# Kernel optimization log

Measured on AMD Instinct MI355X. Metric: run time of the kernel, lower is better.

## Reference

```python
import jax, jax.numpy as jnp
import numpy as np

B, S, D_MODEL, D_QK, D_VO = 4, 2048, 1024, 128, 128
NEG = -1.0e9


def setup_inputs() -> dict:
    key = jax.random.key(0)
    k1, k2, k3, k4, k5 = jax.random.split(key, 5)
    enc = jax.random.normal(k1, (B, S, D_MODEL), dtype=jnp.float32)
    # causal mask: True means masked (masked_fill), broadcast over batch
    causal = jnp.triu(jnp.ones((S, S), dtype=bool), k=1)
    mask = jnp.broadcast_to(causal, (B, S, S))
    scale = 0.02
    W_q = jax.random.normal(k2, (D_MODEL, D_QK), dtype=jnp.float32) * scale
    W_k = jax.random.normal(k3, (D_MODEL, D_QK), dtype=jnp.float32) * scale
    W_v = jax.random.normal(k4, (D_MODEL, D_VO), dtype=jnp.float32) * scale
    W_o = jax.random.normal(k5, (D_VO, D_MODEL), dtype=jnp.float32) * scale
    return {"encodings": enc, "mask": mask, "W_q": W_q, "W_k": W_k, "W_v": W_v, "W_o": W_o}


def reference(encodings, mask, W_q, W_k, W_v, W_o):
    # q,k: [B,S,d_qk]; v: [B,S,d_vo]
    q = jnp.einsum('bsd,de->bse', encodings, W_q)
    k = jnp.einsum('bsd,de->bse', encodings, W_k)
    v = jnp.einsum('bsd,de->bse', encodings, W_v)
    sims = jnp.einsum('bqe,bke->bqk', q, k) / jnp.asarray(D_QK ** 0.5, q.dtype)
    sims = jnp.where(mask, jnp.asarray(NEG, sims.dtype), sims)
    attn = jax.nn.softmax(sims, axis=-1)  # [B,S,S]
    scores = jnp.einsum('bqk,bke->bqe', attn, v)  # [B,S,d_vo]
    return jnp.einsum('bse,ed->bsd', scores, W_o)  # [B,S,d_model]
```

## Files before the change

### kernel.cpp

```cpp
#include <hip/hip_runtime.h>
#include <hip/hip_bf16.h>
#include <stdint.h>

typedef __attribute__((ext_vector_type(8))) short short8;
typedef __attribute__((ext_vector_type(4))) float floatx4;

using bf16 = __hip_bfloat16;

#define SCALE_L2 0.12751793359133147f

__device__ inline unsigned short f2b(float f) {
    bf16 h = __float2bfloat16(f);
    return *(unsigned short*)&h;
}

__global__ __launch_bounds__(256) void prep_all(const float4* __restrict__ enc4,
                                                ushort4* __restrict__ encb4,
                                                const float* __restrict__ Wq,
                                                const float* __restrict__ Wk,
                                                const float* __restrict__ Wv,
                                                const float* __restrict__ Wo,
                                                bf16* __restrict__ Wqkvt,
                                                bf16* __restrict__ Wot) {
    int bx = blockIdx.x;
    if (bx < 8192) {
        int i = bx * 256 + threadIdx.x;
        float4 v = enc4[i];
        ushort4 o;
        o.x = f2b(v.x); o.y = f2b(v.y); o.z = f2b(v.z); o.w = f2b(v.w);
        encb4[i] = o;
    } else {
        int idx = (bx - 8192) * 256 + threadIdx.x;
        int sel = idx >> 17;
        int i = idx & 131071;
        if (sel < 3) {
            const float* W = (sel == 0) ? Wq : (sel == 1) ? Wk : Wv;
            int r = i >> 7, c = i & 127;
            Wqkvt[(size_t)(sel * 128 + c) * 1024 + r] = __float2bfloat16(W[i]);
        } else {
            int r = i >> 10, c = i & 1023;
            Wot[(size_t)c * 128 + r] = __float2bfloat16(Wo[i]);
        }
    }
}

__global__ __launch_bounds__(256) void gemm_qkv64(const bf16* __restrict__ A,
                                                  const bf16* __restrict__ Bt,
                                                  bf16* __restrict__ Qb,
                                                  bf16* __restrict__ Kb,
                                                  bf16* __restrict__ Vtb) {
    __shared__ bf16 As[64 * 40];
    __shared__ bf16 Bs[64 * 40];

    const int tid = threadIdx.x;
    const int m0 = blockIdx.x * 64;
    const int brow0 = blockIdx.y * 64;
    const int proj = brow0 >> 7;
    const int colb = brow0 & 127;
    const int w = tid >> 6, lane = tid & 63;
    const int wm = (w >> 1) * 32, wn = (w & 1) * 32;
    const int quad = lane >> 4, l16 = lane & 15;

    const int ra = tid >> 2, ca = (tid & 3) * 8;

    floatx4 acc[2][2];
#pragma unroll
    for (int i = 0; i < 2; i++)
#pragma unroll
        for (int j = 0; j < 2; j++) acc[i][j] = (floatx4){0.f, 0.f, 0.f, 0.f};

    int4 pa = *(const int4*)&A[(size_t)(m0 + ra) * 1024 + ca];
    int4 pb = *(const int4*)&Bt[(size_t)(brow0 + ra) * 1024 + ca];

    for (int k0 = 0; k0 < 1024; k0 += 32) {
        __syncthreads();
        *(int4*)&As[ra * 40 + ca] = pa;
        *(int4*)&Bs[ra * 40 + ca] = pb;
        __syncthreads();

        if (k0 + 32 < 1024) {
            pa = *(const int4*)&A[(size_t)(m0 + ra) * 1024 + k0 + 32 + ca];
            pb = *(const int4*)&Bt[(size_t)(brow0 + ra) * 1024 + k0 + 32 + ca];
        }

        short8 a[2], b[2];
#pragma unroll
        for (int mt = 0; mt < 2; mt++)
            a[mt] = *(const short8*)&As[(wm + mt * 16 + l16) * 40 + quad * 8];
#pragma unroll
        for (int nt = 0; nt < 2; nt++)
            b[nt] = *(const short8*)&Bs[(wn + nt * 16 + l16) * 40 + quad * 8];
#pragma unroll
        for (int mt = 0; mt < 2; mt++)
#pragma unroll
            for (int nt = 0; nt < 2; nt++)
                acc[mt][nt] = __builtin_amdgcn_mfma_f32_16x16x32_bf16(a[mt], b[nt], acc[mt][nt], 0, 0, 0);
    }

#pragma unroll
    for (int mt = 0; mt < 2; mt++)
#pragma unroll
        for (int nt = 0; nt < 2; nt++)
#pragma unroll
            for (int r = 0; r < 4; r++) {
                int row = m0 + wm + mt * 16 + quad * 4 + r;
                int col = colb + wn + nt * 16 + l16;
                bf16 h = __float2bfloat16(acc[mt][nt][r]);
                if (proj == 0) {
                    Qb[(size_t)row * 128 + col] = h;
                } else if (proj == 1) {
                    Kb[(size_t)row * 128 + col] = h;
                } else {
                    int bb = row >> 11, ss = row & 2047;
                    Vtb[(size_t)bb * 262144 + (size_t)col * 2048 + ss] = h;
                }
            }
}

__global__ __launch_bounds__(256) void gemm_out(const bf16* __restrict__ A,
                                                const bf16* __restrict__ Bt,
                                                float* __restrict__ C) {
    __shared__ bf16 As[64 * 40];
    __shared__ bf16 Bs[128 * 40];

    const int tid = threadIdx.x;
    const int m0 = blockIdx.x * 64;
    const int n0 = blockIdx.y * 128;
    const int w = tid >> 6, lane = tid & 63;
    const int wm = (w >> 1) * 32, wn = (w & 1) * 64;
    const int quad = lane >> 4, l16 = lane & 15;

    const int ra = tid >> 2, ca = (tid & 3) * 8;
    const int rb0 = tid >> 2, rb1 = (tid + 256) >> 2;

    floatx4 acc[2][4];
#pragma unroll
    for (int i = 0; i < 2; i++)
#pragma unroll
        for (int j = 0; j < 4; j++) acc[i][j] = (floatx4){0.f, 0.f, 0.f, 0.f};

    int4 pa  = *(const int4*)&A[(size_t)(m0 + ra) * 128 + ca];
    int4 pb0 = *(const int4*)&Bt[(size_t)(n0 + rb0) * 128 + ca];
    int4 pb1 = *(const int4*)&Bt[(size_t)(n0 + rb1) * 128 + ca];

    for (int k0 = 0; k0 < 128; k0 += 32) {
        __syncthreads();
        *(int4*)&As[ra * 40 + ca] = pa;
        *(int4*)&Bs[rb0 * 40 + ca] = pb0;
        *(int4*)&Bs[rb1 * 40 + ca] = pb1;
        __syncthreads();

        if (k0 + 32 < 128) {
            pa  = *(const int4*)&A[(size_t)(m0 + ra) * 128 + k0 + 32 + ca];
            pb0 = *(const int4*)&Bt[(size_t)(n0 + rb0) * 128 + k0 + 32 + ca];
            pb1 = *(const int4*)&Bt[(size_t)(n0 + rb1) * 128 + k0 + 32 + ca];
        }

        short8 a[2], b[4];
#pragma unroll
        for (int mt = 0; mt < 2; mt++)
            a[mt] = *(const short8*)&As[(wm + mt * 16 + l16) * 40 + quad * 8];
#pragma unroll
        for (int nt = 0; nt < 4; nt++)
            b[nt] = *(const short8*)&Bs[(wn + nt * 16 + l16) * 40 + quad * 8];
#pragma unroll
        for (int mt = 0; mt < 2; mt++)
#pragma unroll
            for (int nt = 0; nt < 4; nt++)
                acc[mt][nt] = __builtin_amdgcn_mfma_f32_16x16x32_bf16(a[mt], b[nt], acc[mt][nt], 0, 0, 0);
    }

#pragma unroll
    for (int mt = 0; mt < 2; mt++)
#pragma unroll
        for (int nt = 0; nt < 4; nt++)
#pragma unroll
            for (int r = 0; r < 4; r++) {
                int row = m0 + wm + mt * 16 + quad * 4 + r;
                int col = n0 + wn + nt * 16 + l16;
                C[(size_t)row * 1024 + col] = acc[mt][nt][r];
            }
}

__global__ __launch_bounds__(256) void flash_split(const bf16* __restrict__ Q,
                                                   const bf16* __restrict__ K,
                                                   const bf16* __restrict__ Vt,
                                                   float* __restrict__ Op,
                                                   float2* __restrict__ Ml) {
    __shared__ bf16 Ps[4 * 16 * 72];

    const int tid = threadIdx.x;
    const int b = blockIdx.x >> 5;
    const int qt = blockIdx.x & 31;
    const int ks = blockIdx.y;
    const int q0 = qt * 64;
    const int w = tid >> 6, lane = tid & 63;
    const int quad = lane >> 4, l16 = lane & 15;

    const int ntiles = qt + 1;
    const int per = (ntiles + 3) >> 2;
    const int start = ks * per;
    const int end = min(start + per, ntiles);

    const int qrow = q0 + w * 16 + l16;
    const bf16* Qrow = &Q[((size_t)b * 2048 + qrow) * 128];
    short8 qf[4];
#pragma unroll
    for (int k4 = 0; k4 < 4; k4++)
        qf[k4] = *(const short8*)&Qrow[k4 * 32 + quad * 8];

    const bf16* Kb = &K[(size_t)b * 2048 * 128];
    const bf16* Vb = &Vt[(size_t)b * 262144];

    float m_run = -1.0e30f, l_run = 0.f;
    floatx4 o[8];
#pragma unroll
    for (int d = 0; d < 8; d++) o[d] = (floatx4){0.f, 0.f, 0.f, 0.f};

    for (int kt = start; kt < end; kt++) {
        const bf16* Kt = Kb + (size_t)(kt * 64) * 128;
        const bf16* Vtt = Vb + kt * 64;

        floatx4 s_acc[4];
#pragma unroll
        for (int nt = 0; nt < 4; nt++) {
            s_acc[nt] = (floatx4){0.f, 0.f, 0.f, 0.f};
#pragma unroll
            for (int k4 = 0; k4 < 4; k4++) {
                short8 kf = *(const short8*)&Kt[(size_t)(nt * 16 + l16) * 128 + k4 * 32 + quad * 8];
                s_acc[nt] = __builtin_amdgcn_mfma_f32_16x16x32_bf16(kf, qf[k4], s_acc[nt], 0, 0, 0);
            }
        }

        float sv[4][4];
#pragma unroll
        for (int nt = 0; nt < 4; nt++)
#pragma unroll
            for (int r = 0; r < 4; r++) {
                float s = s_acc[nt][r] * SCALE_L2;
                if (kt == qt) {
                    int kcol = kt * 64 + nt * 16 + quad * 4 + r;
                    if (kcol > qrow) s = -1.0e9f;
                }
                sv[nt][r] = s;
            }

        float t0 = fmaxf(fmaxf(sv[0][0], sv[0][1]), fmaxf(sv[0][2], sv[0][3]));
        float t1 = fmaxf(fmaxf(sv[1][0], sv[1][1]), fmaxf(sv[1][2], sv[1][3]));
        float t2 = fmaxf(fmaxf(sv[2][0], sv[2][1]), fmaxf(sv[2][2], sv[2][3]));
        float t3 = fmaxf(fmaxf(sv[3][0], sv[3][1]), fmaxf(sv[3][2], sv[3][3]));
        float tmax = fmaxf(fmaxf(t0, t1), fmaxf(t2, t3));
        tmax = fmaxf(tmax, __shfl_xor(tmax, 16));
        tmax = fmaxf(tmax, __shfl_xor(tmax, 32));

        float mnew = fmaxf(m_run, tmax);
        float alpha = exp2f(m_run - mnew);
        m_run = mnew;

        float rsum = 0.f;
#pragma unroll
        for (int nt = 0; nt < 4; nt++)
#pragma unroll
            for (int r = 0; r < 4; r++) {
                float p = exp2f(sv[nt][r] - mnew);
                sv[nt][r] = p;
                rsum += p;
            }
        rsum += __shfl_xor(rsum, 16);
        rsum += __shfl_xor(rsum, 32);
        l_run = l_run * alpha + rsum;

#pragma unroll
        for (int nt = 0; nt < 4; nt++) {
            ushort4 pk;
            pk.x = f2b(sv[nt][0]); pk.y = f2b(sv[nt][1]);
            pk.z = f2b(sv[nt][2]); pk.w = f2b(sv[nt][3]);
            *(ushort4*)&Ps[w * 1152 + l16 * 72 + nt * 16 + quad * 4] = pk;
        }

#pragma unroll
        for (int d = 0; d < 8; d++) {
            o[d][0] *= alpha; o[d][1] *= alpha; o[d][2] *= alpha; o[d][3] *= alpha;
        }

        short8 pf[2];
#pragma unroll
        for (int k2 = 0; k2 < 2; k2++)
            pf[k2] = *(const short8*)&Ps[w * 1152 + l16 * 72 + k2 * 32 + quad * 8];
#pragma unroll
        for (int d = 0; d < 8; d++)
#pragma unroll
            for (int k2 = 0; k2 < 2; k2++) {
                short8 vf = *(const short8*)&Vtt[(size_t)(d * 16 + l16) * 2048 + k2 * 32 + quad * 8];
                o[d] = __builtin_amdgcn_mfma_f32_16x16x32_bf16(vf, pf[k2], o[d], 0, 0, 0);
            }
    }

    const size_t orow = (size_t)ks * 8192 + b * 2048 + qrow;
#pragma unroll
    for (int d = 0; d < 8; d++) {
        float4 v = {o[d][0], o[d][1], o[d][2], o[d][3]};
        *(float4*)&Op[orow * 128 + d * 16 + quad * 4] = v;
    }
    if (lane < 16) Ml[orow] = make_float2(m_run, l_run);
}

__global__ __launch_bounds__(256) void flash_merge(const float* __restrict__ Op,
                                                   const float2* __restrict__ Ml,
                                                   bf16* __restrict__ Sc) {
    int idx = blockIdx.x * 256 + threadIdx.x;
    int row = idx >> 5, dg = (idx & 31) * 4;

    float2 ml[4];
#pragma unroll
    for (int s = 0; s < 4; s++) ml[s] = Ml[(size_t)s * 8192 + row];
    float M = fmaxf(fmaxf(ml[0].x, ml[1].x), fmaxf(ml[2].x, ml[3].x));
    float L = 0.f, wgt[4];
#pragma unroll
    for (int s = 0; s < 4; s++) {
        wgt[s] = exp2f(ml[s].x - M);
        L += ml[s].y * wgt[s];
    }
    float4 acc = {0.f, 0.f, 0.f, 0.f};
#pragma unroll
    for (int s = 0; s < 4; s++) {
        float4 v = *(const float4*)&Op[((size_t)s * 8192 + row) * 128 + dg];
        acc.x += v.x * wgt[s]; acc.y += v.y * wgt[s];
        acc.z += v.z * wgt[s]; acc.w += v.w * wgt[s];
    }
    float inv = 1.0f / L;
    ushort4 o;
    o.x = f2b(acc.x * inv); o.y = f2b(acc.y * inv);
    o.z = f2b(acc.z * inv); o.w = f2b(acc.w * inv);
    *(ushort4*)&Sc[(size_t)row * 128 + dg] = o;
}

extern "C" void kernel_launch(void* const* d_in, const int* in_sizes, int n_in,
                              void* d_out, int out_size, void* d_ws, size_t ws_size,
                              hipStream_t stream) {
    const float* enc = (const float*)d_in[0];
    const float* Wq = (const float*)d_in[2];
    const float* Wk = (const float*)d_in[3];
    const float* Wv = (const float*)d_in[4];
    const float* Wo = (const float*)d_in[5];
    float* out = (float*)d_out;

    const size_t MB = 1024 * 1024;
    char* ws = (char*)d_ws;
    bf16*   encb  = (bf16*)(ws);
    float*  Op    = (float*)(ws);
    bf16*   Qb    = (bf16*)(ws + 16 * MB);
    bf16*   Kb    = (bf16*)(ws + 18 * MB);
    bf16*   Vtb   = (bf16*)(ws + 20 * MB);
    bf16*   Scb   = (bf16*)(ws + 22 * MB);
    bf16*   Wqkvt = (bf16*)(ws + 24 * MB);
    bf16*   Wot   = (bf16*)(ws + 24 * MB + 768 * 1024);
    float2* Ml    = (float2*)(ws + 25 * MB);

    prep_all<<<10240, 256, 0, stream>>>((const float4*)enc, (ushort4*)encb,
                                        Wq, Wk, Wv, Wo, Wqkvt, Wot);

    dim3 blk(256);
    gemm_qkv64<<<dim3(128, 6), blk, 0, stream>>>(encb, Wqkvt, Qb, Kb, Vtb);

    flash_split<<<dim3(128, 4), blk, 0, stream>>>(Qb, Kb, Vtb, Op, Ml);
    flash_merge<<<1024, blk, 0, stream>>>(Op, Ml, Scb);

    gemm_out<<<dim3(128, 8), blk, 0, stream>>>(Scb, Wot, out);
}
```

Baseline: 222.0 us.

## Rebalance flash split-K work, stage K/V in LDS, widen QKV GEMM tiles

The flash kernel now splits the causal work into fixed 4-tile chunks per query tile, giving 576 balanced blocks instead of a 128x4 grid with uneven per-split counts. K and V tiles are staged through shared memory with register prefetch instead of being read directly from global memory. Partial outputs are stored in bf16 to halve merge traffic, and the merge loops over a variable number of chunks. The QKV GEMM uses 64x128 tiles with direct global-to-LDS loads, which drops the register double buffering and LDS padding and may add bank conflicts and precision loss in the partial sums.

Result: faster. 210.9 us (-5.0%).

```diff
diff --git a/kernel.cpp b/kernel.cpp
--- a/kernel.cpp
+++ b/kernel.cpp
@@ -12,6 +12,17 @@
 __device__ inline unsigned short f2b(float f) {
     bf16 h = __float2bfloat16(f);
     return *(unsigned short*)&h;
+}
+__device__ inline float b2f(unsigned short u) {
+    union { unsigned int i; float f; } v;
+    v.i = ((unsigned int)u) << 16;
+    return v.f;
+}
+
+__device__ __forceinline__ void gll16(const bf16* g, bf16* l) {
+    __builtin_amdgcn_global_load_lds((__attribute__((address_space(1))) void*)g,
+                                     (__attribute__((address_space(3))) void*)l,
+                                     16, 0, 0);
 }
 
 __global__ __launch_bounds__(256) void prep_all(const float4* __restrict__ enc4,
@@ -44,71 +55,67 @@
     }
 }
 
-__global__ __launch_bounds__(256) void gemm_qkv64(const bf16* __restrict__ A,
-                                                  const bf16* __restrict__ Bt,
-                                                  bf16* __restrict__ Qb,
-                                                  bf16* __restrict__ Kb,
-                                                  bf16* __restrict__ Vtb) {
-    __shared__ bf16 As[64 * 40];
-    __shared__ bf16 Bs[64 * 40];
+__global__ __launch_bounds__(256) void gemm_qkv(const bf16* __restrict__ A,
+                                                const bf16* __restrict__ Bt,
+                                                bf16* __restrict__ Qb,
+                                                bf16* __restrict__ Kb,
+                                                bf16* __restrict__ Vtb) {
+    __shared__ bf16 As[64 * 32];
+    __shared__ bf16 Bs[128 * 32];
 
     const int tid = threadIdx.x;
     const int m0 = blockIdx.x * 64;
-    const int brow0 = blockIdx.y * 64;
-    const int proj = brow0 >> 7;
-    const int colb = brow0 & 127;
+    const int nsel = blockIdx.y;
+    const int brow0 = nsel * 128;
     const int w = tid >> 6, lane = tid & 63;
-    const int wm = (w >> 1) * 32, wn = (w & 1) * 32;
+    const int wm = (w >> 1) * 32, wn = (w & 1) * 64;
     const int quad = lane >> 4, l16 = lane & 15;
 
-    const int ra = tid >> 2, ca = (tid & 3) * 8;
-
-    floatx4 acc[2][2];
+    const int ar = tid >> 2, akq = (tid & 3) * 8;
+    const int br1 = (tid + 256) >> 2;
+    bf16* As_w  = &As[w * 512];
+    bf16* Bs_w0 = &Bs[w * 512];
+    bf16* Bs_w1 = &Bs[2048 + w * 512];
+
+    floatx4 acc[2][4];
 #pragma unroll
     for (int i = 0; i < 2; i++)
 #pragma unroll
-        for (int j = 0; j < 2; j++) acc[i][j] = (floatx4){0.f, 0.f, 0.f, 0.f};
-
-    int4 pa = *(const int4*)&A[(size_t)(m0 + ra) * 1024 + ca];
-    int4 pb = *(const int4*)&Bt[(size_t)(brow0 + ra) * 1024 + ca];
+        for (int j = 0; j < 4; j++) acc[i][j] = (floatx4){0.f, 0.f, 0.f, 0.f};
 
     for (int k0 = 0; k0 < 1024; k0 += 32) {
         __syncthreads();
-        *(int4*)&As[ra * 40 + ca] = pa;
-        *(int4*)&Bs[ra * 40 + ca] = pb;
-        __syncthreads();
-
-        if (k0 + 32 < 1024) {
-            pa = *(const int4*)&A[(size_t)(m0 + ra) * 1024 + k0 + 32 + ca];
-            pb = *(const int4*)&Bt[(size_t)(brow0 + ra) * 1024 + k0 + 32 + ca];
-        }
-
-        short8 a[2], b[2];
+        gll16(&A[(size_t)(m0 + ar) * 1024 + k0 + akq], As_w);
+        gll16(&Bt[(size_t)(brow0 + ar) * 1024 + k0 + akq], Bs_w0);
+        gll16(&Bt[(size_t)(brow0 + br1) * 1024 + k0 + akq], Bs_w1);
+        __syncthreads();
+
+        short8 a[2], b[4];
 #pragma unroll
         for (int mt = 0; mt < 2; mt++)
-            a[mt] = *(const short8*)&As[(wm + mt * 16 + l16) * 40 + quad * 8];
-#pragma unroll
-        for (int nt = 0; nt < 2; nt++)
-            b[nt] = *(const short8*)&Bs[(wn + nt * 16 + l16) * 40 + quad * 8];
+            a[mt] = *(const short8*)&As[(wm + mt * 16 + l16) * 32 + quad * 8];
+#pragma unroll
+        for (int nt = 0; nt < 4; nt++)
+            b[nt] = *(const short8*)&Bs[(wn + nt * 16 + l16) * 32 + quad * 8];
 #pragma unroll
         for (int mt = 0; mt < 2; mt++)
 #pragma unroll
-            for (int nt = 0; nt < 2; nt++)
+            for (int nt = 0; nt < 4; nt++)
                 acc[mt][nt] = __builtin_amdgcn_mfma_f32_16x16x32_bf16(a[mt], b[nt], acc[mt][nt], 0, 0, 0);
     }
 
 #pragma unroll
     for (int mt = 0; mt < 2; mt++)
 #pragma unroll
-        for (int nt = 0; nt < 2; nt++)
+        for (int nt = 0; nt < 4; nt++)
 #pragma unroll
             for (int r = 0; r < 4; r++) {
                 int row = m0 + wm + mt * 16 + quad * 4 + r;
-                int col = colb + wn + nt * 16 + l16;
+                int col = wn + nt * 16 + l16;
                 bf16 h = __float2bfloat16(acc[mt][nt][r]);
-                if (proj == 0) {
+                if (nsel == 0) {
                     Qb[(size_t)row * 128 + col] = h;
-                } else if (proj == 1) {
+                } else if (nsel == 1) {
                     Kb[(size_t)row * 128 + col] = h;
                 } else {
                     int bb = row >> 11, ss = row & 2047;
@@ -185,22 +192,29 @@
 __global__ __launch_bounds__(256) void flash_split(const bf16* __restrict__ Q,
                                                    const bf16* __restrict__ K,
                                                    const bf16* __restrict__ Vt,
-                                                   float* __restrict__ Op,
+                                                   bf16* __restrict__ Opb,
                                                    float2* __restrict__ Ml) {
+    __shared__ bf16 Ks[64 * 136];
+    __shared__ bf16 Vs[128 * 72];
     __shared__ bf16 Ps[4 * 16 * 72];
 
     const int tid = threadIdx.x;
-    const int b = blockIdx.x >> 5;
-    const int qt = blockIdx.x & 31;
-    const int ks = blockIdx.y;
+    const int x = blockIdx.x;
+    const int b = x / 144;
+    const int id = x - b * 144;
+    const int g = (id >= 112) ? 7 : (id >= 84) ? 6 : (id >= 60) ? 5 : (id >= 40) ? 4
+                : (id >= 24) ? 3 : (id >= 12) ? 2 : (id >= 4) ? 1 : 0;
+    const int nc = g + 1;
+    const int local = id - 2 * g * nc;
+    const int qi = local / nc;
+    const int c = local - qi * nc;
+    const int qt = 4 * g + qi;
     const int q0 = qt * 64;
+    const int start = 4 * c;
+    const int end = min(start + 4, qt + 1);
+
     const int w = tid >> 6, lane = tid & 63;
     const int quad = lane >> 4, l16 = lane & 15;
-
-    const int ntiles = qt + 1;
-    const int per = (ntiles + 3) >> 2;
-    const int start = ks * per;
-    const int end = min(start + per, ntiles);
 
     const int qrow = q0 + w * 16 + l16;
     const bf16* Qrow = &Q[((size_t)b * 2048 + qrow) * 128];
@@ -209,17 +223,39 @@
     for (int k4 = 0; k4 < 4; k4++)
         qf[k4] = *(const short8*)&Qrow[k4 * 32 + quad * 8];
 
-    const bf16* Kb = &K[(size_t)b * 2048 * 128];
-    const bf16* Vb = &Vt[(size_t)b * 262144];
-
     float m_run = -1.0e30f, l_run = 0.f;
     floatx4 o[8];
 #pragma unroll
     for (int d = 0; d < 8; d++) o[d] = (floatx4){0.f, 0.f, 0.f, 0.f};
 
+    int4 kreg[4], vreg[4];
+    const int sr[4]  = {(tid + 0) >> 4, (tid + 256) >> 4, (tid + 512) >> 4, (tid + 768) >> 4};
+    const int scg    = (tid & 15) * 8;
+    const int sr2[4] = {(tid + 0) >> 3, (tid + 256) >> 3, (tid + 512) >> 3, (tid + 768) >> 3};
+    const int scg2   = (tid & 7) * 8;
+
+#pragma unroll
+    for (int i = 0; i < 4; i++) {
+        kreg[i] = *(const int4*)&K[((size_t)b * 2048 + start * 64 + sr[i]) * 128 + scg];
+        vreg[i] = *(const int4*)&Vt[(size_t)b * 262144 + (size_t)sr2[i] * 2048 + start * 64 + scg2];
+    }
+
     for (int kt = start; kt < end; kt++) {
-        const bf16* Kt = Kb + (size_t)(kt * 64) * 128;
-        const bf16* Vtt = Vb + kt * 64;
+        __syncthreads();
+#pragma unroll
+        for (int i = 0; i < 4; i++) {
+            *(int4*)&Ks[sr[i] * 136 + scg] = kreg[i];
+            *(int4*)&Vs[sr2[i] * 72 + scg2] = vreg[i];
+        }
+        __syncthreads();
+
+        if (kt + 1 < end) {
+#pragma unroll
+            for (int i = 0; i < 4; i++) {
+                kreg[i] = *(const int4*)&K[((size_t)b * 2048 + (kt + 1) * 64 + sr[i]) * 128 + scg];
+                vreg[i] = *(const int4*)&Vt[(size_t)b * 262144 + (size_t)sr2[i] * 2048 + (kt + 1) * 64 + scg2];
+            }
+        }
 
         floatx4 s_acc[4];
 #pragma unroll
@@ -227,7 +263,7 @@
             s_acc[nt] = (floatx4){0.f, 0.f, 0.f, 0.f};
 #pragma unroll
             for (int k4 = 0; k4 < 4; k4++) {
-                short8 kf = *(const short8*)&Kt[(size_t)(nt * 16 + l16) * 128 + k4 * 32 + quad * 8];
+                short8 kf = *(const short8*)&Ks[(nt * 16 + l16) * 136 + k4 * 32 + quad * 8];
                 s_acc[nt] = __builtin_amdgcn_mfma_f32_16x16x32_bf16(kf, qf[k4], s_acc[nt], 0, 0, 0);
             }
         }
@@ -291,47 +327,52 @@
         for (int d = 0; d < 8; d++)
 #pragma unroll
             for (int k2 = 0; k2 < 2; k2++) {
-                short8 vf = *(const short8*)&Vtt[(size_t)(d * 16 + l16) * 2048 + k2 * 32 + quad * 8];
+                short8 vf = *(const short8*)&Vs[(d * 16 + l16) * 72 + k2 * 32 + quad * 8];
                 o[d] = __builtin_amdgcn_mfma_f32_16x16x32_bf16(vf, pf[k2], o[d], 0, 0, 0);
             }
     }
 
-    const size_t orow = (size_t)ks * 8192 + b * 2048 + qrow;
+    const int lrow = w * 16 + l16;
+    const size_t obase = ((size_t)x * 64 + lrow) * 128;
 #pragma unroll
     for (int d = 0; d < 8; d++) {
-        float4 v = {o[d][0], o[d][1], o[d][2], o[d][3]};
-        *(float4*)&Op[orow * 128 + d * 16 + quad * 4] = v;
-    }
-    if (lane < 16) Ml[orow] = make_float2(m_run, l_run);
-}
-
-__global__ __launch_bounds__(256) void flash_merge(const float* __restrict__ Op,
+        ushort4 pk;
+        pk.x = f2b(o[d][0]); pk.y = f2b(o[d][1]);
+        pk.z = f2b(o[d][2]); pk.w = f2b(o[d][3]);
+        *(ushort4*)&Opb[obase + d * 16 + quad * 4] = pk;
+    }
+    if (lane < 16) Ml[(size_t)x * 64 + lrow] = make_float2(m_run, l_run);
+}
+
+__global__ __launch_bounds__(256) void flash_merge(const bf16* __restrict__ Opb,
                                                    const float2* __restrict__ Ml,
                                                    bf16* __restrict__ Sc) {
     int idx = blockIdx.x * 256 + threadIdx.x;
     int row = idx >> 5, dg = (idx & 31) * 4;
-
-    float2 ml[4];
-#pragma unroll
-    for (int s = 0; s < 4; s++) ml[s] = Ml[(size_t)s * 8192 + row];
-    float M = fmaxf(fmaxf(ml[0].x, ml[1].x), fmaxf(ml[2].x, ml[3].x));
-    float L = 0.f, wgt[4];
-#pragma unroll
-    for (int s = 0; s < 4; s++) {
-        wgt[s] = exp2f(ml[s].x - M);
-        L += ml[s].y * wgt[s];
-    }
-    float4 acc = {0.f, 0.f, 0.f, 0.f};
-#pragma unroll
-    for (int s = 0; s < 4; s++) {
-        float4 v = *(const float4*)&Op[((size_t)s * 8192 + row) * 128 + dg];
-        acc.x += v.x * wgt[s]; acc.y += v.y * wgt[s];
-        acc.z += v.z * wgt[s]; acc.w += v.w * wgt[s];
+    int b = row >> 11, s = row & 2047;
+    int qt = s >> 6, rl = s & 63;
+    int g = qt >> 2, nc = g + 1;
+    int id0 = b * 144 + 2 * g * nc + (qt & 3) * nc;
+
+    float m[8], l[8], M = -1.0e30f;
+    for (int j = 0; j < nc; j++) {
+        float2 t = Ml[(size_t)(id0 + j) * 64 + rl];
+        m[j] = t.x; l[j] = t.y;
+        M = fmaxf(M, t.x);
+    }
+    float L = 0.f;
+    float a0 = 0.f, a1 = 0.f, a2 = 0.f, a3 = 0.f;
+    for (int j = 0; j < nc; j++) {
+        float wj = exp2f(m[j] - M);
+        L += l[j] * wj;
+        ushort4 p = *(const ushort4*)&Opb[((size_t)(id0 + j) * 64 + rl) * 128 + dg];
+        a0 += wj * b2f(p.x); a1 += wj * b2f(p.y);
+        a2 += wj * b2f(p.z); a3 += wj * b2f(p.w);
     }
     float inv = 1.0f / L;
     ushort4 o;
-    o.x = f2b(acc.x * inv); o.y = f2b(acc.y * inv);
-    o.z = f2b(acc.z * inv); o.w = f2b(acc.w * inv);
+    o.x = f2b(a0 * inv); o.y = f2b(a1 * inv);
+    o.z = f2b(a2 * inv); o.w = f2b(a3 * inv);
     *(ushort4*)&Sc[(size_t)row * 128 + dg] = o;
 }
 
@@ -348,7 +389,7 @@
     const size_t MB = 1024 * 1024;
     char* ws = (char*)d_ws;
     bf16*   encb  = (bf16*)(ws);
-    float*  Op    = (float*)(ws);
+    bf16*   Opb   = (bf16*)(ws);
     bf16*   Qb    = (bf16*)(ws + 16 * MB);
     bf16*   Kb    = (bf16*)(ws + 18 * MB);
     bf16*   Vtb   = (bf16*)(ws + 20 * MB);
@@ -361,10 +402,10 @@
                                         Wq, Wk, Wv, Wo, Wqkvt, Wot);
 
     dim3 blk(256);
-    gemm_qkv64<<<dim3(128, 6), blk, 0, stream>>>(encb, Wqkvt, Qb, Kb, Vtb);
-
-    flash_split<<<dim3(128, 4), blk, 0, stream>>>(Qb, Kb, Vtb, Op, Ml);
-    flash_merge<<<1024, blk, 0, stream>>>(Op, Ml, Scb);
+    gemm_qkv<<<dim3(128, 3), blk, 0, stream>>>(encb, Wqkvt, Qb, Kb, Vtb);
+
+    flash_split<<<576, blk, 0, stream>>>(Qb, Kb, Vtb, Opb, Ml);
+    flash_merge<<<1024, blk, 0, stream>>>(Opb, Ml, Scb);
 
     gemm_out<<<dim3(128, 8), blk, 0, stream>>>(Scb, Wot, out);
 }
```
